# Kernel tuning notes

Hardware: AMD Instinct MI355X
Metric: run time of the kernel (lower is better)

Reference implementation:

```python
import jax, jax.numpy as jnp
import numpy as np

B, P, C, H, W = 2048, 50, 512, 7, 8


def setup_inputs() -> dict:
    key = jax.random.key(0)
    k1, k2 = jax.random.split(key)
    x = jax.random.normal(k1, (B, C, H, W), dtype=jnp.float32)
    # nn.init.xavier_uniform_ on (P, C, H, W) -> small-scale init
    prototype = jax.random.normal(k2, (P, C, H, W), dtype=jnp.float32) * 0.02
    return {"x": x, "prototype": prototype}


def reference(x, prototype):
    """PrototypeLayer euclidean branch.

    Torch original:
      x2_sum = conv2d(x**2, ones_like(prototype))   # full-size kernel -> [B,P,1,1], same value per p
      p2     = sum(prototype**2, dims=(1,2,3)).view(1,P,1,1)
      xp     = conv2d(x, prototype)                  # [B,P,1,1]
      dist   = relu(x2_sum + p2 - 2*xp).view(B,P)
    The full-size-kernel convs reduce to global sums / a [B,P] contraction.
    """
    x2_sum = jnp.sum(x * x, axis=(1, 2, 3))                 # [B]
    p2 = jnp.sum(prototype * prototype, axis=(1, 2, 3))     # [P]
    xp = jnp.einsum('bchw,pchw->bp', x, prototype)          # [B,P]
    distance = jax.nn.relu(x2_sum[:, None] + p2[None, :] - 2.0 * xp)
    return distance
```

## Files before the change

### kernel.cpp

```cpp
#include <hip/hip_runtime.h>
#include <hip/hip_bf16.h>


typedef __bf16 bf16_t;
typedef bf16_t bf16x8 __attribute__((ext_vector_type(8)));
typedef bf16_t bf16x4 __attribute__((ext_vector_type(4)));
typedef float  floatx4 __attribute__((ext_vector_type(4)));

#define KDIM 28672
#define BDIM 2048
#define KSPLIT 32
#define KCHUNK (KDIM / KSPLIT)
#define STEPS (KCHUNK / 64)
#define ASTRIDE 72
#define PREPSPLIT 8
#define PREPCHUNK (KDIM / PREPSPLIT)

__global__ __launch_bounds__(256) void proto_prep(const float* __restrict__ proto,
                                                  bf16_t* __restrict__ pb,
                                                  float* __restrict__ p2p) {
    const int p = blockIdx.x;
    const int kc = blockIdx.y;
    const int t = threadIdx.x;
    float acc = 0.f;
    if (p < 50) {
        const floatx4* src = (const floatx4*)(proto + (long)p * KDIM + kc * PREPCHUNK);
        bf16_t* dst = pb + (long)p * KDIM + kc * PREPCHUNK;
        for (int i = t; i < PREPCHUNK / 4; i += 256) {
            floatx4 v = src[i];
            acc += v[0]*v[0] + v[1]*v[1] + v[2]*v[2] + v[3]*v[3];
            bf16x4 o;
            o[0] = (bf16_t)v[0]; o[1] = (bf16_t)v[1];
            o[2] = (bf16_t)v[2]; o[3] = (bf16_t)v[3];
            *(bf16x4*)(dst + i * 4) = o;
        }
    } else {
        bf16_t* dst = pb + (long)p * KDIM + kc * PREPCHUNK;
        bf16x4 z;
        z[0] = (bf16_t)0.f; z[1] = (bf16_t)0.f; z[2] = (bf16_t)0.f; z[3] = (bf16_t)0.f;
        for (int i = t; i < PREPCHUNK / 4; i += 256)
            *(bf16x4*)(dst + i * 4) = z;
    }
    __shared__ float sred[256];
    sred[t] = acc;
    __syncthreads();
    for (int s = 128; s > 0; s >>= 1) {
        if (t < s) sred[t] += sred[t + s];
        __syncthreads();
    }
    if (t == 0) p2p[kc * 64 + p] = (p < 50) ? sred[0] : 0.f;
}

__global__ __launch_bounds__(256, 4) void proto_main(const float* __restrict__ x,
                                                     const bf16_t* __restrict__ pb,
                                                     float* __restrict__ xpp,
                                                     float* __restrict__ x2p) {
    __shared__ bf16_t As[2][64 * ASTRIDE];

    const int t = threadIdx.x;
    const int lane = t & 63;
    const int wave = t >> 6;
    const int lr = lane & 15;
    const int q  = lane >> 4;
    const int mbase = blockIdx.x * 64;
    const int ks = blockIdx.y;
    const int kbase = ks * KCHUNK;

    const int srow = t >> 2;
    const int sq   = t & 3;
    const float* xrow = x + (long)(mbase + srow) * KDIM + kbase + sq * 16;
    bf16_t* const awr[2] = { &As[0][srow * ASTRIDE + sq * 16],
                             &As[1][srow * ASTRIDE + sq * 16] };

    const int m0 = (wave >> 1) * 32;
    const int n0 = (wave & 1) * 32;
    const bf16_t* pbr0 = pb + (long)(n0 + lr) * KDIM + kbase + q * 8;
    const bf16_t* pbr1 = pb + (long)(n0 + 16 + lr) * KDIM + kbase + q * 8;
    const int ard0 = (m0 + lr) * ASTRIDE + q * 8;
    const int ard1 = (m0 + 16 + lr) * ASTRIDE + q * 8;

    floatx4 acc00 = {0.f,0.f,0.f,0.f};
    floatx4 acc01 = {0.f,0.f,0.f,0.f};
    floatx4 acc10 = {0.f,0.f,0.f,0.f};
    floatx4 acc11 = {0.f,0.f,0.f,0.f};
    float x2acc = 0.f;

    floatx4 c0 = *(const floatx4*)(xrow);
    floatx4 c1 = *(const floatx4*)(xrow + 4);
    floatx4 c2 = *(const floatx4*)(xrow + 8);
    floatx4 c3 = *(const floatx4*)(xrow + 12);
    bf16x8 bc00 = *(const bf16x8*)(pbr0);
    bf16x8 bc01 = *(const bf16x8*)(pbr0 + 32);
    bf16x8 bc10 = *(const bf16x8*)(pbr1);
    bf16x8 bc11 = *(const bf16x8*)(pbr1 + 32);
    {
        x2acc += c0[0]*c0[0] + c0[1]*c0[1] + c0[2]*c0[2] + c0[3]*c0[3]
               + c1[0]*c1[0] + c1[1]*c1[1] + c1[2]*c1[2] + c1[3]*c1[3]
               + c2[0]*c2[0] + c2[1]*c2[1] + c2[2]*c2[2] + c2[3]*c2[3]
               + c3[0]*c3[0] + c3[1]*c3[1] + c3[2]*c3[2] + c3[3]*c3[3];
        bf16x8 lo, hi;
        lo[0]=(bf16_t)c0[0]; lo[1]=(bf16_t)c0[1]; lo[2]=(bf16_t)c0[2]; lo[3]=(bf16_t)c0[3];
        lo[4]=(bf16_t)c1[0]; lo[5]=(bf16_t)c1[1]; lo[6]=(bf16_t)c1[2]; lo[7]=(bf16_t)c1[3];
        hi[0]=(bf16_t)c2[0]; hi[1]=(bf16_t)c2[1]; hi[2]=(bf16_t)c2[2]; hi[3]=(bf16_t)c2[3];
        hi[4]=(bf16_t)c3[0]; hi[5]=(bf16_t)c3[1]; hi[6]=(bf16_t)c3[2]; hi[7]=(bf16_t)c3[3];
        *(bf16x8*)(awr[0])     = lo;
        *(bf16x8*)(awr[0] + 8) = hi;
    }
    c0 = *(const floatx4*)(xrow + 64);
    c1 = *(const floatx4*)(xrow + 68);
    c2 = *(const floatx4*)(xrow + 72);
    c3 = *(const floatx4*)(xrow + 76);
    __syncthreads();

    #pragma unroll 2
    for (int it = 0; it < STEPS; ++it) {
        const int buf = it & 1;

        const int nk1 = (it + 1 < STEPS ? it + 1 : STEPS - 1) * 64;
        bf16x8 bn00 = *(const bf16x8*)(pbr0 + nk1);
        bf16x8 bn01 = *(const bf16x8*)(pbr0 + nk1 + 32);
        bf16x8 bn10 = *(const bf16x8*)(pbr1 + nk1);
        bf16x8 bn11 = *(const bf16x8*)(pbr1 + nk1 + 32);

        const int nk2 = (it + 2 < STEPS ? it + 2 : STEPS - 1) * 64;
        floatx4 n0v = *(const floatx4*)(xrow + nk2);
        floatx4 n1v = *(const floatx4*)(xrow + nk2 + 4);
        floatx4 n2v = *(const floatx4*)(xrow + nk2 + 8);
        floatx4 n3v = *(const floatx4*)(xrow + nk2 + 12);

        if (it + 1 < STEPS) {
            x2acc += c0[0]*c0[0] + c0[1]*c0[1] + c0[2]*c0[2] + c0[3]*c0[3]
                   + c1[0]*c1[0] + c1[1]*c1[1] + c1[2]*c1[2] + c1[3]*c1[3]
                   + c2[0]*c2[0] + c2[1]*c2[1] + c2[2]*c2[2] + c2[3]*c2[3]
                   + c3[0]*c3[0] + c3[1]*c3[1] + c3[2]*c3[2] + c3[3]*c3[3];
            bf16x8 lo, hi;
            lo[0]=(bf16_t)c0[0]; lo[1]=(bf16_t)c0[1]; lo[2]=(bf16_t)c0[2]; lo[3]=(bf16_t)c0[3];
            lo[4]=(bf16_t)c1[0]; lo[5]=(bf16_t)c1[1]; lo[6]=(bf16_t)c1[2]; lo[7]=(bf16_t)c1[3];
            hi[0]=(bf16_t)c2[0]; hi[1]=(bf16_t)c2[1]; hi[2]=(bf16_t)c2[2]; hi[3]=(bf16_t)c2[3];
            hi[4]=(bf16_t)c3[0]; hi[5]=(bf16_t)c3[1]; hi[6]=(bf16_t)c3[2]; hi[7]=(bf16_t)c3[3];
            *(bf16x8*)(awr[buf ^ 1])     = lo;
            *(bf16x8*)(awr[buf ^ 1] + 8) = hi;
        }

        {
            const bf16_t* ab = &As[buf][0];
            bf16x8 a00 = *(const bf16x8*)(ab + ard0);
            bf16x8 a01 = *(const bf16x8*)(ab + ard0 + 32);
            bf16x8 a10 = *(const bf16x8*)(ab + ard1);
            bf16x8 a11 = *(const bf16x8*)(ab + ard1 + 32);
            acc00 = __builtin_amdgcn_mfma_f32_16x16x32_bf16(a00, bc00, acc00, 0, 0, 0);
            acc10 = __builtin_amdgcn_mfma_f32_16x16x32_bf16(a10, bc00, acc10, 0, 0, 0);
            acc01 = __builtin_amdgcn_mfma_f32_16x16x32_bf16(a00, bc10, acc01, 0, 0, 0);
            acc11 = __builtin_amdgcn_mfma_f32_16x16x32_bf16(a10, bc10, acc11, 0, 0, 0);
            acc00 = __builtin_amdgcn_mfma_f32_16x16x32_bf16(a01, bc01, acc00, 0, 0, 0);
            acc10 = __builtin_amdgcn_mfma_f32_16x16x32_bf16(a11, bc01, acc10, 0, 0, 0);
            acc01 = __builtin_amdgcn_mfma_f32_16x16x32_bf16(a01, bc11, acc01, 0, 0, 0);
            acc11 = __builtin_amdgcn_mfma_f32_16x16x32_bf16(a11, bc11, acc11, 0, 0, 0);
        }

        __syncthreads();
        c0 = n0v; c1 = n1v; c2 = n2v; c3 = n3v;
        bc00 = bn00; bc01 = bn01; bc10 = bn10; bc11 = bn11;
    }

    const long base = ((long)ks * BDIM + mbase) * 64;
    #pragma unroll
    for (int r = 0; r < 4; ++r) {
        const int mr = m0 + q * 4 + r;
        xpp[base + (long)mr * 64 + n0 + lr]             = acc00[r];
        xpp[base + (long)mr * 64 + n0 + 16 + lr]        = acc01[r];
        xpp[base + (long)(mr + 16) * 64 + n0 + lr]      = acc10[r];
        xpp[base + (long)(mr + 16) * 64 + n0 + 16 + lr] = acc11[r];
    }

    float* red = (float*)&As[0][0];
    red[t] = x2acc;
    __syncthreads();
    if (t < 64) {
        float s = red[4 * t] + red[4 * t + 1] + red[4 * t + 2] + red[4 * t + 3];
        x2p[ks * BDIM + mbase + t] = s;
    }
}

__global__ __launch_bounds__(256) void proto_finalize(const float* __restrict__ xpp,
                                                      const float* __restrict__ x2p,
                                                      const float* __restrict__ p2p,
                                                      float* __restrict__ out) {
    int idx = blockIdx.x * 256 + threadIdx.x;
    int b = idx >> 6;
    int n = idx & 63;
    if (n >= 50) return;
    float xp = 0.f, x2 = 0.f, p2 = 0.f;
    #pragma unroll
    for (int ksi = 0; ksi < KSPLIT; ++ksi) {
        xp += xpp[((long)ksi * BDIM + b) * 64 + n];
        x2 += x2p[ksi * BDIM + b];
    }
    #pragma unroll
    for (int kc = 0; kc < PREPSPLIT; ++kc)
        p2 += p2p[kc * 64 + n];
    float d = x2 + p2 - 2.f * xp;
    out[b * 50 + n] = d > 0.f ? d : 0.f;
}

extern "C" void kernel_launch(void* const* d_in, const int* in_sizes, int n_in,
                              void* d_out, int out_size, void* d_ws, size_t ws_size,
                              hipStream_t stream) {
    const float* x = (const float*)d_in[0];
    const float* proto = (const float*)d_in[1];
    float* out = (float*)d_out;

    char* ws = (char*)d_ws;
    bf16_t* pb  = (bf16_t*)(ws);
    float*  p2p = (float*)(ws + 3670016);
    float*  x2p = (float*)(ws + 3672064);
    float*  xpp = (float*)(ws + 3934208);

    proto_prep<<<dim3(64, PREPSPLIT), 256, 0, stream>>>(proto, pb, p2p);
    proto_main<<<dim3(32, KSPLIT), 256, 0, stream>>>(x, pb, xpp, x2p);
    proto_finalize<<<(BDIM * 64) / 256, 256, 0, stream>>>(xpp, x2p, p2p, out);
}
```

Before: 340.6 us.

## Pre-swizzle bf16 prototype into MFMA fragment order for contiguous B loads

The prep kernel now writes the bf16 prototype in a tiled layout indexed by K-split, step, half, N-tile and lane, so each 64-lane wave reads one contiguous 1 KB block per fragment. Before, each wave read 16-byte pieces strided by the full K row. This targets poor coalescing and cache-line use on the B-operand global loads in the main GEMM. It adds index arithmetic in the prep kernel and makes the prep writes scattered rather than row-contiguous.

After: 337.2 us. About the same (-1.0%).

```diff
diff --git a/kernel.cpp b/kernel.cpp
--- a/kernel.cpp
+++ b/kernel.cpp
@@ -4,7 +4,6 @@
 
 typedef __bf16 bf16_t;
 typedef bf16_t bf16x8 __attribute__((ext_vector_type(8)));
-typedef bf16_t bf16x4 __attribute__((ext_vector_type(4)));
 typedef float  floatx4 __attribute__((ext_vector_type(4)));
 
 #define KDIM 28672
@@ -17,30 +16,41 @@
 #define PREPCHUNK (KDIM / PREPSPLIT)
 
 __global__ __launch_bounds__(256) void proto_prep(const float* __restrict__ proto,
-                                                  bf16_t* __restrict__ pb,
+                                                  bf16_t* __restrict__ pb2,
                                                   float* __restrict__ p2p) {
     const int p = blockIdx.x;
     const int kc = blockIdx.y;
     const int t = threadIdx.x;
+    const int nt = p >> 4;
+    const int lr = p & 15;
     float acc = 0.f;
-    if (p < 50) {
-        const floatx4* src = (const floatx4*)(proto + (long)p * KDIM + kc * PREPCHUNK);
-        bf16_t* dst = pb + (long)p * KDIM + kc * PREPCHUNK;
-        for (int i = t; i < PREPCHUNK / 4; i += 256) {
-            floatx4 v = src[i];
-            acc += v[0]*v[0] + v[1]*v[1] + v[2]*v[2] + v[3]*v[3];
-            bf16x4 o;
-            o[0] = (bf16_t)v[0]; o[1] = (bf16_t)v[1];
-            o[2] = (bf16_t)v[2]; o[3] = (bf16_t)v[3];
-            *(bf16x4*)(dst + i * 4) = o;
+
+    for (int i = t; i < PREPCHUNK / 8; i += 256) {
+        const int kg = kc * PREPCHUNK + i * 8;
+        bf16x8 o;
+        if (p < 50) {
+            const float* src = proto + (long)p * KDIM + kg;
+            floatx4 v0 = *(const floatx4*)(src);
+            floatx4 v1 = *(const floatx4*)(src + 4);
+            acc += v0[0]*v0[0] + v0[1]*v0[1] + v0[2]*v0[2] + v0[3]*v0[3]
+                 + v1[0]*v1[0] + v1[1]*v1[1] + v1[2]*v1[2] + v1[3]*v1[3];
+            o[0]=(bf16_t)v0[0]; o[1]=(bf16_t)v0[1]; o[2]=(bf16_t)v0[2]; o[3]=(bf16_t)v0[3];
+            o[4]=(bf16_t)v1[0]; o[5]=(bf16_t)v1[1]; o[6]=(bf16_t)v1[2]; o[7]=(bf16_t)v1[3];
+        } else {
+            o[0]=(bf16_t)0.f; o[1]=(bf16_t)0.f; o[2]=(bf16_t)0.f; o[3]=(bf16_t)0.f;
+            o[4]=(bf16_t)0.f; o[5]=(bf16_t)0.f; o[6]=(bf16_t)0.f; o[7]=(bf16_t)0.f;
         }
-    } else {
-        bf16_t* dst = pb + (long)p * KDIM + kc * PREPCHUNK;
-        bf16x4 z;
-        z[0] = (bf16_t)0.f; z[1] = (bf16_t)0.f; z[2] = (bf16_t)0.f; z[3] = (bf16_t)0.f;
-        for (int i = t; i < PREPCHUNK / 4; i += 256)
-            *(bf16x4*)(dst + i * 4) = z;
-    }
+        const int ks   = kg / KCHUNK;
+        const int kr   = kg % KCHUNK;
+        const int step = kr >> 6;
+        const int ko   = kr & 63;
+        const int h    = ko >> 5;
+        const int q    = (ko & 31) >> 3;
+        const long addr = (long)(ks * STEPS + step) * 4096 + h * 2048
+                        + nt * 512 + (q * 16 + lr) * 8;
+        *(bf16x8*)(pb2 + addr) = o;
+    }
+
     __shared__ float sred[256];
     sred[t] = acc;
     __syncthreads();
@@ -52,7 +62,7 @@
 }
 
 __global__ __launch_bounds__(256, 4) void proto_main(const float* __restrict__ x,
-                                                     const bf16_t* __restrict__ pb,
+                                                     const bf16_t* __restrict__ pb2,
                                                      float* __restrict__ xpp,
                                                      float* __restrict__ x2p) {
     __shared__ bf16_t As[2][64 * ASTRIDE];
@@ -74,8 +84,8 @@
 
     const int m0 = (wave >> 1) * 32;
     const int n0 = (wave & 1) * 32;
-    const bf16_t* pbr0 = pb + (long)(n0 + lr) * KDIM + kbase + q * 8;
-    const bf16_t* pbr1 = pb + (long)(n0 + 16 + lr) * KDIM + kbase + q * 8;
+    const int t0 = (wave & 1) * 2;
+    const bf16_t* bbase = pb2 + (long)ks * STEPS * 4096 + lane * 8;
     const int ard0 = (m0 + lr) * ASTRIDE + q * 8;
     const int ard1 = (m0 + 16 + lr) * ASTRIDE + q * 8;
 
@@ -89,10 +99,10 @@
     floatx4 c1 = *(const floatx4*)(xrow + 4);
     floatx4 c2 = *(const floatx4*)(xrow + 8);
     floatx4 c3 = *(const floatx4*)(xrow + 12);
-    bf16x8 bc00 = *(const bf16x8*)(pbr0);
-    bf16x8 bc01 = *(const bf16x8*)(pbr0 + 32);
-    bf16x8 bc10 = *(const bf16x8*)(pbr1);
-    bf16x8 bc11 = *(const bf16x8*)(pbr1 + 32);
+    bf16x8 bc00 = *(const bf16x8*)(bbase + t0 * 512);
+    bf16x8 bc01 = *(const bf16x8*)(bbase + 2048 + t0 * 512);
+    bf16x8 bc10 = *(const bf16x8*)(bbase + (t0 + 1) * 512);
+    bf16x8 bc11 = *(const bf16x8*)(bbase + 2048 + (t0 + 1) * 512);
     {
         x2acc += c0[0]*c0[0] + c0[1]*c0[1] + c0[2]*c0[2] + c0[3]*c0[3]
                + c1[0]*c1[0] + c1[1]*c1[1] + c1[2]*c1[2] + c1[3]*c1[3]
@@ -116,11 +126,12 @@
     for (int it = 0; it < STEPS; ++it) {
         const int buf = it & 1;
 
-        const int nk1 = (it + 1 < STEPS ? it + 1 : STEPS - 1) * 64;
-        bf16x8 bn00 = *(const bf16x8*)(pbr0 + nk1);
-        bf16x8 bn01 = *(const bf16x8*)(pbr0 + nk1 + 32);
-        bf16x8 bn10 = *(const bf16x8*)(pbr1 + nk1);
-        bf16x8 bn11 = *(const bf16x8*)(pbr1 + nk1 + 32);
+        const int n1 = (it + 1 < STEPS ? it + 1 : STEPS - 1);
+        const bf16_t* bp = bbase + n1 * 4096;
+        bf16x8 bn00 = *(const bf16x8*)(bp + t0 * 512);
+        bf16x8 bn01 = *(const bf16x8*)(bp + 2048 + t0 * 512);
+        bf16x8 bn10 = *(const bf16x8*)(bp + (t0 + 1) * 512);
+        bf16x8 bn11 = *(const bf16x8*)(bp + 2048 + (t0 + 1) * 512);
 
         const int nk2 = (it + 2 < STEPS ? it + 2 : STEPS - 1) * 64;
         floatx4 n0v = *(const floatx4*)(xrow + nk2);
@@ -211,12 +222,12 @@
     float* out = (float*)d_out;
 
     char* ws = (char*)d_ws;
-    bf16_t* pb  = (bf16_t*)(ws);
+    bf16_t* pb2 = (bf16_t*)(ws);
     float*  p2p = (float*)(ws + 3670016);
     float*  x2p = (float*)(ws + 3672064);
     float*  xpp = (float*)(ws + 3934208);
 
-    proto_prep<<<dim3(64, PREPSPLIT), 256, 0, stream>>>(proto, pb, p2p);
-    proto_main<<<dim3(32, KSPLIT), 256, 0, stream>>>(x, pb, xpp, x2p);
+    proto_prep<<<dim3(64, PREPSPLIT), 256, 0, stream>>>(proto, pb2, p2p);
+    proto_main<<<dim3(32, KSPLIT), 256, 0, stream>>>(x, pb2, xpp, x2p);
     proto_finalize<<<(BDIM * 64) / 256, 256, 0, stream>>>(xpp, x2p, p2p, out);
 }
```
